# Kernel optimization log

Hardware: AMD Instinct MI355X
Metric: run time of the kernel (lower is better)

The kernel has to match this reference:

```python
import jax, jax.numpy as jnp
import numpy as np

K = 3          # kernel_size
STRIDE = 1
PAD = 1
BASIS = 8      # act_fun.get_size() (Hermite basis order)


def _unfold(x):
    # x: [B, Cin, H, W] -> patches [B, Cin, K*K, L] (same ordering as F.unfold)
    b, c, h, w = x.shape
    p = jax.lax.conv_general_dilated_patches(
        x, filter_shape=(K, K), window_strides=(STRIDE, STRIDE),
        padding=[(PAD, PAD), (PAD, PAD)])
    # p: [B, Cin*K*K, Hout, Wout], channel-major ordering (Cin, Kh, Kw)
    ho, wo = p.shape[2], p.shape[3]
    return p.reshape(b, c, K * K, ho * wo), ho, wo


def _hermite(x):
    # Physicists' Hermite polynomials H_0..H_{BASIS-1}, stacked on last axis.
    hs = [jnp.ones_like(x), 2.0 * x]
    for n in range(1, BASIS - 1):
        hs.append(2.0 * x * hs[n] - 2.0 * n * hs[n - 1])
    return jnp.stack(hs[:BASIS], axis=-1)


def setup_inputs() -> dict:
    key = jax.random.key(0)
    k1, k2, k3, k4 = jax.random.split(key, 4)
    cin, cout = 64, 128
    x = jax.random.normal(k1, (16, cin, 32, 32), dtype=jnp.float32)
    # xavier_normal on [Cin,Cout,K^2,1]: std = sqrt(2/(fan_in+fan_out)) over last two dims -> use small randn
    w_b = jax.random.normal(k2, (cin, cout, K * K, 1), dtype=jnp.float32)
    w_s = jax.random.normal(k3, (cin, cout, K * K, 1), dtype=jnp.float32) * 0.001
    c = jax.random.normal(k4, (cin, cout, K * K, 1, BASIS), dtype=jnp.float32) * 0.1
    return {"x": x, "w_b": w_b, "w_s": w_s, "c": c}


def reference(x, w_b, w_s, c):
    b = x.shape[0]
    xw, ho, wo = _unfold(x)                      # [B, Cin, K2, L]
    phi = _hermite(xw)                           # [B, Cin, K2, L, BASIS]
    res = jax.nn.silu(xw)                        # residual activation
    # effective spline weight: w_s * c, contracted over Cin, K2, basis
    cw = w_s[..., 0, None] * c[:, :, :, 0, :]    # [Cin, Cout, K2, BASIS]
    out = (jnp.einsum('ioka,bikla->bol', cw, phi)
           + jnp.einsum('iok,bikl->bol', w_b[..., 0], res))  # [B, Cout, L]
    return out.reshape(b, -1, ho, wo)
```

## Files before the change

kernel.cpp:

```cpp
#include <hip/hip_runtime.h>
#include <stdint.h>

typedef unsigned short ushort_t;
typedef short short8 __attribute__((ext_vector_type(8)));
typedef float f32x4 __attribute__((ext_vector_type(4)));

#define CIN   64
#define COUT  128
#define BATCH 16
#define LPIX  1024
#define NTOT  (BATCH*LPIX)
#define C2N   576
#define PIXN  (BATCH*34*34)
#define NSTEP2 72
#define KS    4
#define PART_ELEMS (NTOT*COUT)
#define FEAT_BLOCKS (PIXN/4)
#define WPREP_BLOCKS 32

#define FEAT_BYTES (PIXN*C2N*2)
#define W_OFF      FEAT_BYTES
#define W_BYTES    (COUT*NSTEP2*64*2)
#define BIAS_OFF   (W_OFF + W_BYTES)
#define PART_OFF   (BIAS_OFF + 512)
#define PART_BYTES (PART_ELEMS*2)
#define WS_NEED    ((size_t)PART_OFF + (size_t)(KS-1)*PART_BYTES)

#define WAITVM(n) asm volatile("s_waitcnt vmcnt(" #n ")" ::: "memory")
#define BAR() __builtin_amdgcn_s_barrier()

__device__ __forceinline__ ushort_t to_bf16(float f) {
  union { float f; uint32_t u; } v; v.f = f;
  uint32_t r = (v.u + 0x7fffu + ((v.u >> 16) & 1u)) >> 16;
  return (ushort_t)r;
}
__device__ __forceinline__ float from_bf16(ushort_t u) {
  union { uint32_t u; float f; } v; v.u = ((uint32_t)u) << 16;
  return v.f;
}

__device__ __forceinline__ void basis9(float x, float* o) {
  float hm = 1.f, h = 2.f * x;
  o[0] = hm; o[1] = h;
#pragma unroll
  for (int n = 1; n < 7; ++n) {
    float nx = 2.f * x * h - 2.f * (float)n * hm;
    hm = h; h = nx;
    o[n + 1] = nx;
  }
  o[8] = x / (1.f + __expf(-x));
}

__device__ __forceinline__ void load16(const void* g, void* l) {
  __builtin_amdgcn_global_load_lds(
      (const __attribute__((address_space(1))) uint32_t*)g,
      (__attribute__((address_space(3))) uint32_t*)l, 16, 0, 0);
}

__global__ void prep_kernel(const float* __restrict__ x, ushort_t* __restrict__ feat,
                            const float* __restrict__ wb, const float* __restrict__ wsp,
                            const float* __restrict__ cc, ushort_t* __restrict__ W,
                            float* __restrict__ bias) {
  __shared__ ushort_t wl[4][NSTEP2 * 64 + 16];
  __shared__ float bl[16];
  const int t = threadIdx.x;
  if (blockIdx.x < FEAT_BLOCKS) {
    const int lane = t & 63;
    const int pg = blockIdx.x * 4 + (t >> 6);
    const int xx = pg % 34;
    const int rest = pg / 34;
    const int yy = rest % 34;
    const int bb = rest / 34;
    float v = 0.f;
    if (xx >= 1 && xx <= 32 && yy >= 1 && yy <= 32)
      v = x[((bb * CIN + lane) * 32 + (yy - 1)) * 32 + (xx - 1)];
    float o[9];
    basis9(v, o);
    ushort_t* dst = feat + (size_t)pg * C2N + lane;
#pragma unroll
    for (int f = 1; f < 9; ++f) dst[f * 64] = to_bf16(o[f]);
  } else {
    const int mg = blockIdx.x - FEAT_BLOCKS;
    const int i = t >> 2;
    const int mq = t & 3;
    const int m = mg * 4 + mq;
    const int base = (i * COUT + m) * 9;
    const int r = ((((i >> 3) & 7) ^ (m & 7)) << 3) | (i & 7);
    float h0 = 0.f;
#pragma unroll
    for (int kk = 0; kk < 9; ++kk) {
      const float ws_ = wsp[base + kk];
      const float wbv = wb[base + kk];
      const float* cp = cc + (size_t)(base + kk) * 8;
      h0 += ws_ * cp[0];
#pragma unroll
      for (int sf = 1; sf <= 8; ++sf) {
        const float val = (sf < 8) ? ws_ * cp[sf] : wbv;
        wl[mq][((sf - 1) * 9 + kk) * 64 + r] = to_bf16(val);
      }
    }
#pragma unroll
    for (int off = 4; off < 64; off <<= 1) h0 += __shfl_down(h0, off, 64);
    if ((t & 63) < 4) bl[(t >> 6) * 4 + (t & 3)] = h0;
    __syncthreads();
    if (t < 4) bias[mg * 4 + t] = bl[t] + bl[4 + t] + bl[8 + t] + bl[12 + t];
#pragma unroll 4
    for (int jj = 0; jj < 36; ++jj) {
      const int flat = jj * 256 + t;
      const int row = flat >> 5, col = flat & 31;
      const int mq2 = row / NSTEP2, s2 = row - mq2 * NSTEP2;
      const uint32_t v = *(const uint32_t*)&wl[mq2][s2 * 64 + col * 2];
      *(uint32_t*)&W[(size_t)(mg * 4 + mq2) * (NSTEP2 * 64) + s2 * 64 + col * 2] = v;
    }
  }
}

__global__ __launch_bounds__(256, 2) void gemm_kernel(const ushort_t* __restrict__ feat,
                                                      const ushort_t* __restrict__ W,
                                                      const float* __restrict__ bias,
                                                      float* __restrict__ out,
                                                      ushort_t* __restrict__ part) {
  __shared__ ushort_t Ab[4][4096];
  __shared__ ushort_t Hb[2720 * 8];
  const int t = threadIdx.x;
  const int lane = t & 63;
  const int wn = t >> 6;

  const int logical = (blockIdx.x & 7) * 64 + (blockIdx.x >> 3);
  const int nb = logical >> 3;
  const int rem = logical & 7;
  const int mt = rem >> 2;
  const int ksplit = rem & 3;
  const int lo = ksplit * 18;

  const int b  = nb >> 2;
  const int y0 = (nb & 3) * 8;
  const int pixbase = (b * 34 + y0) * 34;

  const char* Wb = (const char*)W + mt * 64 * (NSTEP2 * 64 * 2);
  const char* Fb = (const char*)feat;

  f32x4 acc[4][4];
#pragma unroll
  for (int a = 0; a < 4; ++a)
#pragma unroll
    for (int c = 0; c < 4; ++c) acc[a][c] = (f32x4)0.f;

  auto stage_halo = [&](int c2s) {
    const char* base = Fb + (size_t)pixbase * (C2N * 2) + (c2s + 1) * 128;
#pragma unroll
    for (int it = 0; it < 11; ++it) {
      const int q = it * 256 + t;
      if (q < 2720) {
        const int L = q >> 3;
        const int sl = (q & 7) ^ (L & 7);
        load16(base + L * (C2N * 2) + (sl << 4), &Hb[q * 8]);
      }
    }
  };

  auto stageA = [&](int p, int s) {
#pragma unroll
    for (int q = 0; q < 2; ++q) {
      const int idx16 = q * 256 + t;
      const int m = idx16 >> 3, ccn = idx16 & 7;
      load16(Wb + m * (NSTEP2 * 64 * 2) + s * 128 + ccn * 16, &Ab[p][idx16 * 8]);
    }
  };

  auto compute = [&](int p, int j) {
    const int dy = j / 3, dx = j - dy * 3;
#pragma unroll
    for (int ks = 0; ks < 2; ++ks) {
      short8 av[4], bv[4];
      const int kslot = ks * 4 + (lane >> 4);
#pragma unroll
      for (int mf = 0; mf < 4; ++mf) {
        const int row = mf * 16 + (lane & 15);
        av[mf] = *(const short8*)&Ab[p][row * 64 + ((kslot ^ (row & 7)) << 3)];
      }
#pragma unroll
      for (int nf = 0; nf < 4; ++nf) {
        const int nl = wn * 64 + nf * 16 + (lane & 15);
        const int L = ((nl >> 5) + dy) * 34 + (nl & 31) + dx;
        bv[nf] = *(const short8*)&Hb[L * 64 + ((kslot ^ (L & 7)) << 3)];
      }
      __builtin_amdgcn_s_setprio(1);
#pragma unroll
      for (int mf = 0; mf < 4; ++mf)
#pragma unroll
        for (int nf = 0; nf < 4; ++nf)
          acc[mf][nf] = __builtin_amdgcn_mfma_f32_16x16x32_bf16(av[mf], bv[nf],
                                                                acc[mf][nf], 0, 0, 0);
      __builtin_amdgcn_s_setprio(0);
    }
  };

#define GSTEP(j, N)                                         \
  {                                                         \
    if ((j) + 2 < 18) stageA(((j) + 2) & 3, lo + (j) + 2);  \
    WAITVM(N);                                              \
    BAR();                                                  \
    compute((j) & 3, (j) % 9);                              \
  }

  stage_halo(2 * ksplit);
  stageA(0, lo);
  stageA(1, lo + 1);

  GSTEP(0, 4);  GSTEP(1, 4);  GSTEP(2, 4);  GSTEP(3, 4);  GSTEP(4, 4);
  GSTEP(5, 4);  GSTEP(6, 4);  GSTEP(7, 4);  GSTEP(8, 4);

  BAR();
  stage_halo(2 * ksplit + 1);

  GSTEP(9, 2);  GSTEP(10, 4); GSTEP(11, 4); GSTEP(12, 4); GSTEP(13, 4);
  GSTEP(14, 4); GSTEP(15, 4); GSTEP(16, 2); GSTEP(17, 0);
#undef GSTEP

  if (ksplit) {
    ushort_t* dst = part + (size_t)(ksplit - 1) * PART_ELEMS;
#pragma unroll
    for (int mf = 0; mf < 4; ++mf)
#pragma unroll
      for (int rg = 0; rg < 4; ++rg) {
        const int m = mt * 64 + mf * 16 + (lane >> 4) * 4 + rg;
#pragma unroll
        for (int nf = 0; nf < 4; ++nf) {
          const int n = nb * 256 + wn * 64 + nf * 16 + (lane & 15);
          const int bb = n >> 10, ll = n & 1023;
          dst[(bb * COUT + m) * LPIX + ll] = to_bf16(acc[mf][nf][rg]);
        }
      }
  } else {
#pragma unroll
    for (int mf = 0; mf < 4; ++mf)
#pragma unroll
      for (int rg = 0; rg < 4; ++rg) {
        const int m = mt * 64 + mf * 16 + (lane >> 4) * 4 + rg;
        const float bv = bias[m];
#pragma unroll
        for (int nf = 0; nf < 4; ++nf) {
          const int n = nb * 256 + wn * 64 + nf * 16 + (lane & 15);
          const int bb = n >> 10, ll = n & 1023;
          out[(bb * COUT + m) * LPIX + ll] = acc[mf][nf][rg] + bv;
        }
      }
  }
}

__global__ void add_kernel(float* __restrict__ out, const ushort_t* __restrict__ part) {
  const int i = (blockIdx.x * 256 + threadIdx.x) * 8;
  f32x4 a0 = *(const f32x4*)&out[i];
  f32x4 a1 = *(const f32x4*)&out[i + 4];
#pragma unroll
  for (int j = 0; j < KS - 1; ++j) {
    const short8 pv = *(const short8*)&part[(size_t)j * PART_ELEMS + i];
#pragma unroll
    for (int e = 0; e < 4; ++e) {
      a0[e] += from_bf16((ushort_t)pv[e]);
      a1[e] += from_bf16((ushort_t)pv[e + 4]);
    }
  }
  *(f32x4*)&out[i] = a0;
  *(f32x4*)&out[i + 4] = a1;
}

__global__ void naive_kernel(const float* __restrict__ x, const float* __restrict__ wb,
                             const float* __restrict__ wsp, const float* __restrict__ cc,
                             float* __restrict__ out) {
  const int idx = blockIdx.x * 256 + threadIdx.x;
  if (idx >= BATCH * COUT * LPIX) return;
  const int l = idx & 1023, o = (idx >> 10) & 127, b = idx >> 17;
  const int h = l >> 5, w = l & 31;
  float acc = 0.f;
  for (int i = 0; i < CIN; ++i)
    for (int kk = 0; kk < 9; ++kk) {
      const int yy = h + kk / 3 - 1, xx = w + kk % 3 - 1;
      const float v = (yy >= 0 && yy < 32 && xx >= 0 && xx < 32)
                          ? x[((b * CIN + i) * 32 + yy) * 32 + xx] : 0.f;
      float ftr[9];
      basis9(v, ftr);
      const int base = (i * COUT + o) * 9 + kk;
      const float* cp = cc + base * 8;
      float dot = 0.f;
#pragma unroll
      for (int f = 0; f < 8; ++f) dot += cp[f] * ftr[f];
      acc += wsp[base] * dot + wb[base] * ftr[8];
    }
  out[idx] = acc;
}

extern "C" void kernel_launch(void* const* d_in, const int* in_sizes, int n_in,
                              void* d_out, int out_size, void* d_ws, size_t ws_size,
                              hipStream_t stream) {
  const float* x  = (const float*)d_in[0];
  const float* wb = (const float*)d_in[1];
  const float* wsp = (const float*)d_in[2];
  const float* cc = (const float*)d_in[3];
  float* out = (float*)d_out;

  if (ws_size < WS_NEED) {
    naive_kernel<<<(BATCH * COUT * LPIX + 255) / 256, 256, 0, stream>>>(x, wb, wsp, cc, out);
    return;
  }

  char* ws = (char*)d_ws;
  ushort_t* feat = (ushort_t*)ws;
  ushort_t* W    = (ushort_t*)(ws + W_OFF);
  float* bias    = (float*)(ws + BIAS_OFF);
  ushort_t* part = (ushort_t*)(ws + PART_OFF);

  prep_kernel<<<FEAT_BLOCKS + WPREP_BLOCKS, 256, 0, stream>>>(x, feat, wb, wsp, cc, W, bias);
  gemm_kernel<<<64 * 2 * KS, 256, 0, stream>>>(feat, W, bias, out, part);
  add_kernel<<<PART_ELEMS / 2048, 256, 0, stream>>>(out, part);
}
```

Baseline: 45.55 us.

## Widen GEMM tile to full Cout and split K eight ways

Each GEMM block now covers all 128 output channels with a 2x2 wave layout and 4x8 MFMA accumulators per wave, so the halo-staged feature tile is reused across both M halves. The K dimension is split eight ways instead of four, giving one halo stage per block and 9 steps with double-buffered weight tiles. This removes the duplicate halo loads across M tiles but doubles the bf16 partial buffers that add_kernel must read back, and raises register pressure from 128 accumulator floats per thread, which may hurt occupancy at launch bounds (256,2).

Result: slower. 49.28 us (+8.2%).

```diff
diff --git a/kernel.cpp b/kernel.cpp
--- a/kernel.cpp
+++ b/kernel.cpp
@@ -13,7 +13,7 @@
 #define C2N   576
 #define PIXN  (BATCH*34*34)
 #define NSTEP2 72
-#define KS    4
+#define KS    8
 #define PART_ELEMS (NTOT*COUT)
 #define FEAT_BLOCKS (PIXN/4)
 #define WPREP_BLOCKS 32
@@ -120,34 +120,32 @@
                                                       const float* __restrict__ bias,
                                                       float* __restrict__ out,
                                                       ushort_t* __restrict__ part) {
-  __shared__ ushort_t Ab[4][4096];
+  __shared__ ushort_t Ab[2][8192];
   __shared__ ushort_t Hb[2720 * 8];
   const int t = threadIdx.x;
   const int lane = t & 63;
-  const int wn = t >> 6;
+  const int wave = t >> 6;
+  const int wm = wave >> 1, wn = wave & 1;
 
   const int logical = (blockIdx.x & 7) * 64 + (blockIdx.x >> 3);
   const int nb = logical >> 3;
-  const int rem = logical & 7;
-  const int mt = rem >> 2;
-  const int ksplit = rem & 3;
-  const int lo = ksplit * 18;
+  const int ksplit = logical & 7;
 
   const int b  = nb >> 2;
   const int y0 = (nb & 3) * 8;
   const int pixbase = (b * 34 + y0) * 34;
 
-  const char* Wb = (const char*)W + mt * 64 * (NSTEP2 * 64 * 2);
+  const char* Wb = (const char*)W;
   const char* Fb = (const char*)feat;
 
-  f32x4 acc[4][4];
+  f32x4 acc[4][8];
 #pragma unroll
   for (int a = 0; a < 4; ++a)
 #pragma unroll
-    for (int c = 0; c < 4; ++c) acc[a][c] = (f32x4)0.f;
-
-  auto stage_halo = [&](int c2s) {
-    const char* base = Fb + (size_t)pixbase * (C2N * 2) + (c2s + 1) * 128;
+    for (int c = 0; c < 8; ++c) acc[a][c] = (f32x4)0.f;
+
+  {
+    const char* base = Fb + (size_t)pixbase * (C2N * 2) + (ksplit + 1) * 128;
 #pragma unroll
     for (int it = 0; it < 11; ++it) {
       const int q = it * 256 + t;
@@ -157,11 +155,12 @@
         load16(base + L * (C2N * 2) + (sl << 4), &Hb[q * 8]);
       }
     }
-  };
-
-  auto stageA = [&](int p, int s) {
-#pragma unroll
-    for (int q = 0; q < 2; ++q) {
+  }
+
+  auto stageA = [&](int p, int j) {
+    const int s = ksplit * 9 + j;
+#pragma unroll
+    for (int q = 0; q < 4; ++q) {
       const int idx16 = q * 256 + t;
       const int m = idx16 >> 3, ccn = idx16 & 7;
       load16(Wb + m * (NSTEP2 * 64 * 2) + s * 128 + ccn * 16, &Ab[p][idx16 * 8]);
@@ -172,16 +171,16 @@
     const int dy = j / 3, dx = j - dy * 3;
 #pragma unroll
     for (int ks = 0; ks < 2; ++ks) {
-      short8 av[4], bv[4];
+      short8 av[4], bv[8];
       const int kslot = ks * 4 + (lane >> 4);
 #pragma unroll
       for (int mf = 0; mf < 4; ++mf) {
-        const int row = mf * 16 + (lane & 15);
+        const int row = wm * 64 + mf * 16 + (lane & 15);
         av[mf] = *(const short8*)&Ab[p][row * 64 + ((kslot ^ (row & 7)) << 3)];
       }
 #pragma unroll
-      for (int nf = 0; nf < 4; ++nf) {
-        const int nl = wn * 64 + nf * 16 + (lane & 15);
+      for (int nf = 0; nf < 8; ++nf) {
+        const int nl = wn * 128 + nf * 16 + (lane & 15);
         const int L = ((nl >> 5) + dy) * 34 + (nl & 31) + dx;
         bv[nf] = *(const short8*)&Hb[L * 64 + ((kslot ^ (L & 7)) << 3)];
       }
@@ -189,33 +188,24 @@
 #pragma unroll
       for (int mf = 0; mf < 4; ++mf)
 #pragma unroll
-        for (int nf = 0; nf < 4; ++nf)
+        for (int nf = 0; nf < 8; ++nf)
           acc[mf][nf] = __builtin_amdgcn_mfma_f32_16x16x32_bf16(av[mf], bv[nf],
                                                                 acc[mf][nf], 0, 0, 0);
       __builtin_amdgcn_s_setprio(0);
     }
   };
 
-#define GSTEP(j, N)                                         \
+  stageA(0, 0);
+#define GSTEP(j)                                            \
   {                                                         \
-    if ((j) + 2 < 18) stageA(((j) + 2) & 3, lo + (j) + 2);  \
-    WAITVM(N);                                              \
-    BAR();                                                  \
-    compute((j) & 3, (j) % 9);                              \
-  }
-
-  stage_halo(2 * ksplit);
-  stageA(0, lo);
-  stageA(1, lo + 1);
-
-  GSTEP(0, 4);  GSTEP(1, 4);  GSTEP(2, 4);  GSTEP(3, 4);  GSTEP(4, 4);
-  GSTEP(5, 4);  GSTEP(6, 4);  GSTEP(7, 4);  GSTEP(8, 4);
-
-  BAR();
-  stage_halo(2 * ksplit + 1);
-
-  GSTEP(9, 2);  GSTEP(10, 4); GSTEP(11, 4); GSTEP(12, 4); GSTEP(13, 4);
-  GSTEP(14, 4); GSTEP(15, 4); GSTEP(16, 2); GSTEP(17, 0);
+    BAR();          \
+    if ((j) + 1 < 9) stageA(((j) + 1) & 1, (j) + 1);        \
+    if ((j) + 1 < 9) { WAITVM(4); } else { WAITVM(0); }     \
+    BAR();           \
+    compute((j) & 1, (j));                                  \
+  }
+  GSTEP(0); GSTEP(1); GSTEP(2); GSTEP(3); GSTEP(4);
+  GSTEP(5); GSTEP(6); GSTEP(7); GSTEP(8);
 #undef GSTEP
 
   if (ksplit) {
@@ -224,10 +214,10 @@
     for (int mf = 0; mf < 4; ++mf)
 #pragma unroll
       for (int rg = 0; rg < 4; ++rg) {
-        const int m = mt * 64 + mf * 16 + (lane >> 4) * 4 + rg;
-#pragma unroll
-        for (int nf = 0; nf < 4; ++nf) {
-          const int n = nb * 256 + wn * 64 + nf * 16 + (lane & 15);
+        const int m = wm * 64 + mf * 16 + (lane >> 4) * 4 + rg;
+#pragma unroll
+        for (int nf = 0; nf < 8; ++nf) {
+          const int n = nb * 256 + wn * 128 + nf * 16 + (lane & 15);
           const int bb = n >> 10, ll = n & 1023;
           dst[(bb * COUT + m) * LPIX + ll] = to_bf16(acc[mf][nf][rg]);
         }
@@ -237,11 +227,11 @@
     for (int mf = 0; mf < 4; ++mf)
 #pragma unroll
       for (int rg = 0; rg < 4; ++rg) {
-        const int m = mt * 64 + mf * 16 + (lane >> 4) * 4 + rg;
+        const int m = wm * 64 + mf * 16 + (lane >> 4) * 4 + rg;
         const float bv = bias[m];
 #pragma unroll
-        for (int nf = 0; nf < 4; ++nf) {
-          const int n = nb * 256 + wn * 64 + nf * 16 + (lane & 15);
+        for (int nf = 0; nf < 8; ++nf) {
+          const int n = nb * 256 + wn * 128 + nf * 16 + (lane & 15);
           const int bb = n >> 10, ll = n & 1023;
           out[(bb * COUT + m) * LPIX + ll] = acc[mf][nf][rg] + bv;
         }
@@ -312,6 +302,6 @@
   ushort_t* part = (ushort_t*)(ws + PART_OFF);
 
   prep_kernel<<<FEAT_BLOCKS + WPREP_BLOCKS, 256, 0, stream>>>(x, feat, wb, wsp, cc, W, bias);
-  gemm_kernel<<<64 * 2 * KS, 256, 0, stream>>>(feat, W, bias, out, part);
+  gemm_kernel<<<64 * KS, 256, 0, stream>>>(feat, W, bias, out, part);
   add_kernel<<<PART_ELEMS / 2048, 256, 0, stream>>>(out, part);
 }
```
